# Performance work log

Measured on AMD Instinct MI355X. Metric: run time of the kernel, lower is better.

The kernel has to match this reference:

```python
import jax, jax.numpy as jnp
import numpy as np

K = 2  # num_selected_experts
NOISE_STD = 1.0

def setup_inputs() -> dict:
    key = jax.random.key(0)
    k1, k2, k3, k4 = jax.random.split(key, 4)
    G, S, H, E = 32, 1024, 2048, 64
    tokens = jax.random.normal(k1, (G, S, H), dtype=jnp.float32)
    noise = jax.random.normal(k2, (G * S, E), dtype=jnp.float32) * NOISE_STD
    # nn.Linear(H, E): weight (E, H), bias (E); kaiming-uniform-ish scale
    lim = 1.0 / np.sqrt(H)
    W = jax.random.uniform(k3, (E, H), dtype=jnp.float32, minval=-lim, maxval=lim)
    b = jax.random.uniform(k4, (E,), dtype=jnp.float32, minval=-lim, maxval=lim)
    return {"tokens": tokens, "noise": noise, "W": W, "b": b}

def reference(tokens, noise, W, b):
    G, S, H = tokens.shape
    E = W.shape[0]
    flat = tokens.reshape(G * S, H)
    # linear projection + pre-sampled gaussian noise (training mode)
    logits = jnp.einsum('nh,eh->ne', flat, W) + b + noise  # (G*S, E)
    probs = jax.nn.softmax(logits, axis=-1)
    kk = min(K, E)
    topk_vals, topk_idx = jax.lax.top_k(probs, kk)  # (G*S, k)
    topk_w = topk_vals / (topk_vals.sum(axis=-1, keepdims=True) + 1e-9)
    # aux loss stats over experts
    importance = probs.sum(axis=0)                     # (E,)
    load = (probs > 0).astype(jnp.float32).sum(axis=0) # (E,)
    aux_loss = jnp.var(importance * load, ddof=1) * 0.01  # torch .var() is unbiased
    return (topk_idx.reshape(G, S, kk),
            topk_w.reshape(G, S, kk),
            aux_loss,
            probs.reshape(G, S, E))
```

## Files before the change

kernel.cpp:

```cpp
#include <hip/hip_runtime.h>


constexpr int GS    = 32768;
constexpr int EXPN  = 64;
constexpr int HID   = 2048;
constexpr int BM    = 64;
constexpr int KHALF = 1024;
constexpr int NSUB  = KHALF / 32;
constexpr int NCH   = KHALF / 64;
constexpr int BUFB  = 16384;

typedef __attribute__((ext_vector_type(8))) short s16x8;
typedef __attribute__((ext_vector_type(4))) float f32x4;

#define AS_GLOBAL(p) ((const __attribute__((address_space(1))) void*)(p))
#define AS_LDS(p)    ((__attribute__((address_space(3))) void*)(p))

__device__ __forceinline__ void decomp8(float4 x0, float4 x1, s16x8& h, s16x8& m)
{
    float v[8] = {x0.x,x0.y,x0.z,x0.w,x1.x,x1.y,x1.z,x1.w};
    #pragma unroll
    for (int i = 0; i < 8; ++i) {
        union { float f; unsigned u; } a; a.f = v[i];
        unsigned hb = (a.u + 0x7fffu + ((a.u >> 16) & 1u)) >> 16;
        union { unsigned u; float f; } hf; hf.u = hb << 16;
        float r = (v[i] - hf.f) * 256.f;
        union { float f; unsigned u; } rb; rb.f = r;
        h[i] = (short)hb;
        m[i] = (short)(rb.u >> 16);
    }
}

__device__ __forceinline__ unsigned short f2bf(float x) {
    union { float f; unsigned u; } v; v.f = x;
    return (unsigned short)((v.u + 0x7fffu + ((v.u >> 16) & 1u)) >> 16);
}

__global__ __launch_bounds__(256)
void prep_kernel(const float* __restrict__ W, short* __restrict__ WhF,
                 float* __restrict__ ws)
{
    if (blockIdx.x == 0 && threadIdx.x < 2 * EXPN)
        ws[threadIdx.x] = 0.f;

    const int t  = blockIdx.x * 256 + threadIdx.x;
    const int cs = t >> 8;
    const int nt = (t >> 6) & 3;
    const int l  = t & 63;
    const int e  = nt * 16 + (l & 15);
    const int kb = cs * 32 + ((l >> 4) << 3);
    const float* p = W + (size_t)e * HID + kb;
    float4 x0 = *(const float4*)p;
    float4 x1 = *(const float4*)(p + 4);
    float v[8] = {x0.x,x0.y,x0.z,x0.w,x1.x,x1.y,x1.z,x1.w};
    s16x8 h;
    #pragma unroll
    for (int i = 0; i < 8; ++i) h[i] = (short)f2bf(v[i]);
    *(s16x8*)&WhF[(size_t)t * 8] = h;
}

__global__ __launch_bounds__(512, 2)
void router_kernel(const float* __restrict__ tokens,
                   const float* __restrict__ noise,
                   const float* __restrict__ bias,
                   const short* __restrict__ WhF,
                   float* __restrict__ out,
                   float* __restrict__ ws)
{
    __shared__ __align__(16) char smem[2 * BUFB];

    const int tid  = threadIdx.x;
    const int lane = tid & 63;
    const int wv   = tid >> 6;
    const int mt   = wv & 3;
    const int kh   = wv >> 2;
    const int row0 = blockIdx.x * BM;

    const float* Ap = tokens
        + (size_t)(row0 + mt * 16 + (lane & 15)) * HID
        + kh * KHALF + ((lane >> 4) << 3);

    auto stage = [&](int b, int c) {
        char* base = smem + b * BUFB;
        #pragma unroll
        for (int i = 0; i < 2; ++i) {
            const int r    = wv * 2 + i;
            const int half = r >> 3;
            const int sub  = (r >> 2) & 1;
            const int nt   = r & 3;
            const int cs   = half * NSUB + c * 2 + sub;
            const short* src = WhF + ((size_t)cs * 256 + nt * 64 + lane) * 8;
            __builtin_amdgcn_global_load_lds(AS_GLOBAL(src),
                                             AS_LDS(base + r * 1024), 16, 0, 0);
        }
    };

    f32x4 accM[4], accS[4];
    #pragma unroll
    for (int nt = 0; nt < 4; ++nt) { accM[nt] = (f32x4)0.f; accS[nt] = (f32x4)0.f; }

    float4 aA0 = *(const float4*)(Ap);
    float4 aA1 = *(const float4*)(Ap + 4);
    float4 aA2 = *(const float4*)(Ap + 32);
    float4 aA3 = *(const float4*)(Ap + 36);
    float4 aB0, aB1, aB2, aB3;
    stage(0, 0);
    __syncthreads();

#define CHUNK(A0, A1, A2, A3, N0, N1, N2, N3, c)                                   \
    {                                                                              \
        const int bc = (c) & 1;                                                    \
        if ((c) + 1 < NCH) {                                                       \
            stage(bc ^ 1, (c) + 1);                                                \
            N0 = *(const float4*)(Ap + ((c) + 1) * 64);                            \
            N1 = *(const float4*)(Ap + ((c) + 1) * 64 + 4);                        \
            N2 = *(const float4*)(Ap + ((c) + 1) * 64 + 32);                       \
            N3 = *(const float4*)(Ap + ((c) + 1) * 64 + 36);                       \
        }                                                                          \
        const char* wb = smem + bc * BUFB + kh * 8192;                             \
        s16x8 ah, am;                                                              \
        decomp8(A0, A1, ah, am);                                                   \
        _Pragma("unroll")                                                          \
        for (int nt = 0; nt < 4; ++nt) {                                           \
            s16x8 bh = *(const s16x8*)(wb + nt * 1024 + lane * 16);                \
            accM[nt] = __builtin_amdgcn_mfma_f32_16x16x32_bf16(ah, bh, accM[nt], 0, 0, 0); \
            accS[nt] = __builtin_amdgcn_mfma_f32_16x16x32_bf16(am, bh, accS[nt], 0, 0, 0); \
        }                                                                          \
        decomp8(A2, A3, ah, am);                                                   \
        _Pragma("unroll")                                                          \
        for (int nt = 0; nt < 4; ++nt) {                                           \
            s16x8 bh = *(const s16x8*)(wb + 4096 + nt * 1024 + lane * 16);         \
            accM[nt] = __builtin_amdgcn_mfma_f32_16x16x32_bf16(ah, bh, accM[nt], 0, 0, 0); \
            accS[nt] = __builtin_amdgcn_mfma_f32_16x16x32_bf16(am, bh, accS[nt], 0, 0, 0); \
        }                                                                          \
        __syncthreads();              \
    }

    for (int c = 0; c < NCH; c += 2) {
        CHUNK(aA0, aA1, aA2, aA3, aB0, aB1, aB2, aB3, c);
        CHUNK(aB0, aB1, aB2, aB3, aA0, aA1, aA2, aA3, c + 1);
    }
#undef CHUNK

    float (*lg)[EXPN + 1] = (float (*)[EXPN + 1])smem;
    float (*red)[EXPN]    = (float (*)[EXPN])(smem + BM * (EXPN + 1) * 4);

    if (kh == 0) {
        #pragma unroll
        for (int nt = 0; nt < 4; ++nt)
            #pragma unroll
            for (int r = 0; r < 4; ++r)
                lg[mt * 16 + (lane >> 4) * 4 + r][nt * 16 + (lane & 15)]
                    = accM[nt][r] + 0.00390625f * accS[nt][r];
    }
    __syncthreads();
    if (kh == 1) {
        #pragma unroll
        for (int nt = 0; nt < 4; ++nt)
            #pragma unroll
            for (int r = 0; r < 4; ++r)
                lg[mt * 16 + (lane >> 4) * 4 + r][nt * 16 + (lane & 15)]
                    += accM[nt][r] + 0.00390625f * accS[nt][r];
    }
    __syncthreads();

    float* out_idx   = out;
    float* out_w     = out + 2 * GS;
    float* out_probs = out + 4 * GS + 1;

    const float blane = bias[lane];
    float impL = 0.f, cntL = 0.f;

    for (int rr = 0; rr < 8; ++rr) {
        const int r = (wv << 3) + rr;
        const size_t row = (size_t)row0 + r;
        float v = lg[r][lane] + blane + noise[row * EXPN + lane];

        float m = v;
        #pragma unroll
        for (int off = 32; off >= 1; off >>= 1)
            m = fmaxf(m, __shfl_xor(m, off));
        float e = expf(v - m);
        float s = e;
        #pragma unroll
        for (int off = 32; off >= 1; off >>= 1)
            s += __shfl_xor(s, off);
        float p = e / s;

        out_probs[row * EXPN + lane] = p;
        impL += p;
        cntL += (p > 0.f) ? 1.f : 0.f;

        float v1 = p; int i1 = lane;
        #pragma unroll
        for (int off = 32; off >= 1; off >>= 1) {
            float ov = __shfl_xor(v1, off);
            int   oi = __shfl_xor(i1, off);
            if (ov > v1 || (ov == v1 && oi < i1)) { v1 = ov; i1 = oi; }
        }
        float v2 = (lane == i1) ? -1.f : p; int i2 = lane;
        #pragma unroll
        for (int off = 32; off >= 1; off >>= 1) {
            float ov = __shfl_xor(v2, off);
            int   oi = __shfl_xor(i2, off);
            if (ov > v2 || (ov == v2 && oi < i2)) { v2 = ov; i2 = oi; }
        }
        if (lane == 0) {
            float denom = v1 + v2 + 1e-9f;
            out_idx[row * 2 + 0] = (float)i1;
            out_idx[row * 2 + 1] = (float)i2;
            out_w[row * 2 + 0] = v1 / denom;
            out_w[row * 2 + 1] = v2 / denom;
        }
    }

    red[wv][lane]     = impL;
    red[8 + wv][lane] = cntL;
    __syncthreads();
    if (tid < EXPN) {
        float t1 = 0.f, t2 = 0.f;
        #pragma unroll
        for (int w = 0; w < 8; ++w) { t1 += red[w][tid]; t2 += red[8 + w][tid]; }
        atomicAdd(&ws[tid], t1);
        atomicAdd(&ws[EXPN + tid], t2);
    }
}

__global__ void aux_kernel(const float* __restrict__ ws, float* __restrict__ out)
{
    const int lane = threadIdx.x;
    float x = ws[lane] * ws[EXPN + lane];
    float s = x;
    #pragma unroll
    for (int off = 32; off >= 1; off >>= 1)
        s += __shfl_xor(s, off);
    float mean = s * (1.f / 64.f);
    float d = x - mean;
    float ss = d * d;
    #pragma unroll
    for (int off = 32; off >= 1; off >>= 1)
        ss += __shfl_xor(ss, off);
    if (lane == 0)
        out[4 * GS] = 0.01f * (ss / 63.f);
}

extern "C" void kernel_launch(void* const* d_in, const int* in_sizes, int n_in,
                              void* d_out, int out_size, void* d_ws, size_t ws_size,
                              hipStream_t stream)
{
    const float* tokens = (const float*)d_in[0];
    const float* noise  = (const float*)d_in[1];
    const float* W      = (const float*)d_in[2];
    const float* bias   = (const float*)d_in[3];
    float* out = (float*)d_out;
    float* ws  = (float*)d_ws;

    short* WhF = (short*)(ws + 128);

    prep_kernel<<<EXPN * HID / 8 / 256, 256, 0, stream>>>(W, WhF, ws);
    router_kernel<<<GS / BM, 512, 0, stream>>>(tokens, noise, bias, WhF,
                                               out, ws);
    aux_kernel<<<1, 64, 0, stream>>>(ws, out);
}
```

Baseline: 78.74 us.

## Double row tile to 128 with 1024-thread blocks and fuse aux loss via last-block

Each block now handles 128 token rows with 16 waves, so every staged weight chunk in LDS is shared by twice as many rows and the number of blocks is halved. The separate aux-loss kernel is removed: a global atomic counter picks the last block to finish, which computes the variance after a threadfence, saving one kernel launch. The cost is one block per CU at 1024 threads, which reduces latency hiding, plus an extra atomic and fences per block. The logits LDS row padding changes to 66 floats.

```diff
diff --git a/kernel.cpp b/kernel.cpp
--- a/kernel.cpp
+++ b/kernel.cpp
@@ -4,11 +4,14 @@
 constexpr int GS    = 32768;
 constexpr int EXPN  = 64;
 constexpr int HID   = 2048;
-constexpr int BM    = 64;
+constexpr int BM    = 128;
 constexpr int KHALF = 1024;
 constexpr int NSUB  = KHALF / 32;
 constexpr int NCH   = KHALF / 64;
 constexpr int BUFB  = 16384;
+constexpr int LGB   = BM * (EXPN + 2) * 4;
+constexpr int SMEMB = (2 * BUFB > LGB + 32 * EXPN * 4) ? 2 * BUFB
+                                                       : LGB + 32 * EXPN * 4;
 
 typedef __attribute__((ext_vector_type(8))) short s16x8;
 typedef __attribute__((ext_vector_type(4))) float f32x4;
@@ -40,7 +43,7 @@
 void prep_kernel(const float* __restrict__ W, short* __restrict__ WhF,
                  float* __restrict__ ws)
 {
-    if (blockIdx.x == 0 && threadIdx.x < 2 * EXPN)
+    if (blockIdx.x == 0 && threadIdx.x < 2 * EXPN + 1)
         ws[threadIdx.x] = 0.f;
 
     const int t  = blockIdx.x * 256 + threadIdx.x;
@@ -59,7 +62,7 @@
     *(s16x8*)&WhF[(size_t)t * 8] = h;
 }
 
-__global__ __launch_bounds__(512, 2)
+__global__ __launch_bounds__(1024, 1)
 void router_kernel(const float* __restrict__ tokens,
                    const float* __restrict__ noise,
                    const float* __restrict__ bias,
@@ -67,13 +70,14 @@
                    float* __restrict__ out,
                    float* __restrict__ ws)
 {
-    __shared__ __align__(16) char smem[2 * BUFB];
+    __shared__ __align__(16) char smem[SMEMB];
+    __shared__ int lastFlag;
 
     const int tid  = threadIdx.x;
     const int lane = tid & 63;
     const int wv   = tid >> 6;
-    const int mt   = wv & 3;
-    const int kh   = wv >> 2;
+    const int mt   = wv & 7;
+    const int kh   = wv >> 3;
     const int row0 = blockIdx.x * BM;
 
     const float* Ap = tokens
@@ -82,17 +86,13 @@
 
     auto stage = [&](int b, int c) {
         char* base = smem + b * BUFB;
-        #pragma unroll
-        for (int i = 0; i < 2; ++i) {
-            const int r    = wv * 2 + i;
-            const int half = r >> 3;
-            const int sub  = (r >> 2) & 1;
-            const int nt   = r & 3;
-            const int cs   = half * NSUB + c * 2 + sub;
-            const short* src = WhF + ((size_t)cs * 256 + nt * 64 + lane) * 8;
-            __builtin_amdgcn_global_load_lds(AS_GLOBAL(src),
-                                             AS_LDS(base + r * 1024), 16, 0, 0);
-        }
+        const int half = wv >> 3;
+        const int sub  = (wv >> 2) & 1;
+        const int nt   = wv & 3;
+        const int cs   = half * NSUB + c * 2 + sub;
+        const short* src = WhF + ((size_t)cs * 256 + nt * 64 + lane) * 8;
+        __builtin_amdgcn_global_load_lds(AS_GLOBAL(src),
+                                         AS_LDS(base + wv * 1024), 16, 0, 0);
     };
 
     f32x4 accM[4], accS[4];
@@ -142,8 +142,8 @@
     }
 #undef CHUNK
 
-    float (*lg)[EXPN + 1] = (float (*)[EXPN + 1])smem;
-    float (*red)[EXPN]    = (float (*)[EXPN])(smem + BM * (EXPN + 1) * 4);
+    float (*lg)[EXPN + 2] = (float (*)[EXPN + 2])smem;
+    float (*red)[EXPN]    = (float (*)[EXPN])(smem + LGB);
 
     if (kh == 0) {
         #pragma unroll
@@ -214,34 +214,39 @@
         }
     }
 
-    red[wv][lane]     = impL;
-    red[8 + wv][lane] = cntL;
+    red[wv][lane]      = impL;
+    red[16 + wv][lane] = cntL;
     __syncthreads();
     if (tid < EXPN) {
         float t1 = 0.f, t2 = 0.f;
         #pragma unroll
-        for (int w = 0; w < 8; ++w) { t1 += red[w][tid]; t2 += red[8 + w][tid]; }
+        for (int w = 0; w < 16; ++w) { t1 += red[w][tid]; t2 += red[16 + w][tid]; }
         atomicAdd(&ws[tid], t1);
         atomicAdd(&ws[EXPN + tid], t2);
     }
-}
-
-__global__ void aux_kernel(const float* __restrict__ ws, float* __restrict__ out)
-{
-    const int lane = threadIdx.x;
-    float x = ws[lane] * ws[EXPN + lane];
-    float s = x;
-    #pragma unroll
-    for (int off = 32; off >= 1; off >>= 1)
-        s += __shfl_xor(s, off);
-    float mean = s * (1.f / 64.f);
-    float d = x - mean;
-    float ss = d * d;
-    #pragma unroll
-    for (int off = 32; off >= 1; off >>= 1)
-        ss += __shfl_xor(ss, off);
-    if (lane == 0)
-        out[4 * GS] = 0.01f * (ss / 63.f);
+
+    __threadfence();
+    if (tid == 0) {
+        unsigned prev = atomicAdd((unsigned*)&ws[2 * EXPN], 1u);
+        lastFlag = (prev == (unsigned)(gridDim.x - 1)) ? 1 : 0;
+    }
+    __syncthreads();
+    if (lastFlag && wv == 0) {
+        __threadfence();
+        float x = ws[lane] * ws[EXPN + lane];
+        float s = x;
+        #pragma unroll
+        for (int off = 32; off >= 1; off >>= 1)
+            s += __shfl_xor(s, off);
+        float mean = s * (1.f / 64.f);
+        float d = x - mean;
+        float ss = d * d;
+        #pragma unroll
+        for (int off = 32; off >= 1; off >>= 1)
+            ss += __shfl_xor(ss, off);
+        if (lane == 0)
+            out[4 * GS] = 0.01f * (ss / 63.f);
+    }
 }
 
 extern "C" void kernel_launch(void* const* d_in, const int* in_sizes, int n_in,
@@ -255,10 +260,9 @@
     float* out = (float*)d_out;
     float* ws  = (float*)d_ws;
 
-    short* WhF = (short*)(ws + 128);
+    short* WhF = (short*)(ws + 130);
 
     prep_kernel<<<EXPN * HID / 8 / 256, 256, 0, stream>>>(W, WhF, ws);
-    router_kernel<<<GS / BM, 512, 0, stream>>>(tokens, noise, bias, WhF,
-                                               out, ws);
-    aux_kernel<<<1, 64, 0, stream>>>(ws, out);
-}
+    router_kernel<<<GS / BM, 1024, 0, stream>>>(tokens, noise, bias, WhF,
+                                                out, ws);
+}
```

Result: slower. 146.3 us (+85.8%).
